# Performance work log

Hardware: AMD Instinct MI355X
Metric: run time of the kernel (lower is better)

The kernel has to match this reference:

```python
import jax, jax.numpy as jnp
import numpy as np
from fractions import Fraction
from math import factorial

# irreps metadata for "32x0e + 16x1o + 8x2e" (in/out) and "0e + 1o + 2e" (edge)
# parity of each irrep here equals (-1)**l, so parity selection == (l1+l2+l3) even
IRR_IN = [(32, 0), (16, 1), (8, 2)]   # (multiplicity, l)
IRR_SH = [(1, 0), (1, 1), (1, 2)]
IRR_OUT = IRR_IN

def _offsets(irr):
    offs, o = [], 0
    for mul, l in irr:
        offs.append(o)
        o += mul * (2 * l + 1)
    return offs, o

OFF_IN, DIM_IN = _offsets(IRR_IN)    # DIM_IN = 120
OFF_SH, DIM_SH = _offsets(IRR_SH)    # DIM_SH = 9
OFF_OUT, DIM_OUT = _offsets(IRR_OUT)

def _su2_cg(j1, j2, j3):
    """SU(2) Clebsch-Gordan tensor (e3nn convention), integer l."""
    f = factorial
    C = np.zeros((2 * j1 + 1, 2 * j2 + 1, 2 * j3 + 1))
    for m1 in range(-j1, j1 + 1):
        for m2 in range(-j2, j2 + 1):
            m3 = m1 + m2
            if abs(m3) > j3:
                continue
            vmin = max(-j1 + j2 + m3, -j1 + m1, 0)
            vmax = min(j2 + j3 + m1, j3 - j1 + j2, j3 + m3)
            c = ((2 * j3 + 1) * Fraction(
                f(j3 + j1 - j2) * f(j3 - j1 + j2) * f(j1 + j2 - j3) * f(j3 + m3) * f(j3 - m3),
                f(j1 + j2 + j3 + 1) * f(j1 - m1) * f(j1 + m1) * f(j2 - m2) * f(j2 + m2))) ** 0.5
            S = Fraction(0)
            for v in range(vmin, vmax + 1):
                S += (-1) ** (v + j2 + m2) * Fraction(
                    f(j2 + j3 + m1 - v) * f(j1 - m1 + v),
                    f(v) * f(j3 - j1 + j2 - v) * f(j3 + m3 - v) * f(v + j1 - j2 - m3))
            C[j1 + m1, j2 + m2, j3 + m3] = float(c) * float(S)
    return C

def _q(l):
    """real->complex change of basis for real spherical harmonics (e3nn)."""
    q = np.zeros((2 * l + 1, 2 * l + 1), dtype=np.complex128)
    for m in range(-l, 0):
        q[l + m, l - m] = 1 / np.sqrt(2)
        q[l + m, l + m] = -1j / np.sqrt(2)
    q[l, l] = 1
    for m in range(1, l + 1):
        q[l + m, l + m] = (-1) ** m / np.sqrt(2)
        q[l + m, l - m] = 1j * (-1) ** m / np.sqrt(2)
    return ((-1j) ** l) * q

def _w3j(l1, l2, l3):
    """real-basis Wigner 3j tensor, unit Frobenius norm (e3nn o3.wigner_3j)."""
    C = _su2_cg(l1, l2, l3).astype(np.complex128)
    C = np.einsum('ij,kl,mn,ikn->jlm', _q(l1), _q(l2), np.conj(_q(l3)).T, C)
    C = np.real(C)
    return (C / np.linalg.norm(C)).astype(np.float32)

# build 'uvw' instructions exactly as FullyConnectedTensorProduct does
INSTR = []
_wo = 0
for _i1, (_m1, _l1) in enumerate(IRR_IN):
    for _i2, (_m2, _l2) in enumerate(IRR_SH):
        for _i3, (_m3, _l3) in enumerate(IRR_OUT):
            if abs(_l1 - _l2) <= _l3 <= _l1 + _l2 and (_l1 + _l2 + _l3) % 2 == 0:
                INSTR.append(dict(i1=_i1, i2=_i2, i3=_i3, wo=_wo, cg=_w3j(_l1, _l2, _l3)))
                _wo += _m1 * _m2 * _m3
WEIGHT_NUMEL = _wo  # 3456

# path_normalization='element', irrep_normalization='component':
# coeff = sqrt((2*l_out+1) / sum_{paths into out} mul1*mul2)
_FAN = {}
for _ins in INSTR:
    _FAN[_ins['i3']] = _FAN.get(_ins['i3'], 0) + IRR_IN[_ins['i1']][0] * IRR_SH[_ins['i2']][0]
for _ins in INSTR:
    _l3 = IRR_OUT[_ins['i3']][1]
    _ins['coeff'] = float(np.sqrt((2 * _l3 + 1) / _FAN[_ins['i3']]))


def _tensor_product(x1, x2, w):
    """x1 (E,120) gathered node feats, x2 (E,9) edge SH, w (E,3456) radial weights."""
    E = x1.shape[0]
    acc = [None] * len(IRR_OUT)
    for ins in INSTR:
        m1, l1 = IRR_IN[ins['i1']]
        m3, l3 = IRR_OUT[ins['i3']]
        d1, d2 = 2 * l1 + 1, 2 * IRR_SH[ins['i2']][1] + 1
        x1b = x1[:, OFF_IN[ins['i1']]:OFF_IN[ins['i1']] + m1 * d1].reshape(E, m1, d1)
        x2b = x2[:, OFF_SH[ins['i2']]:OFF_SH[ins['i2']] + d2]        # mul2 == 1
        wb = w[:, ins['wo']:ins['wo'] + m1 * m3].reshape(E, m1, m3)
        cg = jnp.asarray(ins['cg'])                                   # (d1,d2,d3)
        tmp = jnp.einsum('eui,ej,ijk->euk', x1b, x2b, cg)             # (E,m1,d3)
        c = ins['coeff'] * jnp.einsum('euk,euw->ewk', tmp, wb)        # (E,m3,d3)
        acc[ins['i3']] = c if acc[ins['i3']] is None else acc[ins['i3']] + c
    return jnp.concatenate([a.reshape(E, -1) for a in acc], axis=-1)


def _self_interaction(agg, si_ws):
    """o3.Linear: per-l channel mixing, scaled by 1/sqrt(fan_in)."""
    N = agg.shape[0]
    outs = []
    for (m, l), off, W in zip(IRR_OUT, OFF_OUT, si_ws):
        d = 2 * l + 1
        xb = agg[:, off:off + m * d].reshape(N, m, d)
        outs.append((jnp.einsum('nuk,uv->nvk', xb, W) * (1.0 / np.sqrt(m))).reshape(N, -1))
    return jnp.concatenate(outs, axis=-1)


def setup_inputs() -> dict:
    key = jax.random.key(0)
    ks = jax.random.split(key, 10)
    N, E, NB = 4096, 32768, 8
    return {
        'node_features': jax.random.normal(ks[0], (N, DIM_IN), jnp.float32),
        'edge_index': jax.random.randint(ks[1], (2, E), 0, N, dtype=jnp.int32),
        'edge_sh': jax.random.normal(ks[2], (E, DIM_SH), jnp.float32),
        'edge_radial': jax.random.uniform(ks[3], (E, NB), dtype=jnp.float32),
        'w1': jax.random.normal(ks[4], (NB, 64), jnp.float32) / np.sqrt(NB),
        'b1': jnp.zeros((64,), jnp.float32),
        'w2': jax.random.normal(ks[5], (64, 64), jnp.float32) / np.sqrt(64),
        'b2': jnp.zeros((64,), jnp.float32),
        'w3': jax.random.normal(ks[6], (64, WEIGHT_NUMEL), jnp.float32) / np.sqrt(64),
        'b3': jnp.zeros((WEIGHT_NUMEL,), jnp.float32),
        'si_w0': jax.random.normal(ks[7], (32, 32), jnp.float32),
        'si_w1': jax.random.normal(ks[8], (16, 16), jnp.float32),
        'si_w2': jax.random.normal(ks[9], (8, 8), jnp.float32),
    }


def reference(node_features, edge_index, edge_sh, edge_radial,
              w1, b1, w2, b2, w3, b3, si_w0, si_w1, si_w2):
    src, dst = edge_index[0], edge_index[1]
    # radial MLP -> per-edge tensor-product weights
    h = jax.nn.silu(edge_radial @ w1 + b1)
    h = jax.nn.silu(h @ w2 + b2)
    weights = h @ w3 + b3                                     # (E, 3456)
    # gather-TP-scatter message passing
    msgs = _tensor_product(node_features[src], edge_sh, weights)   # (E, 120)
    agg = jax.ops.segment_sum(msgs, dst, num_segments=node_features.shape[0])
    out = _self_interaction(agg, [si_w0, si_w1, si_w2])
    return out + node_features  # shapes match -> residual
```

## Files before the change

kernel.cpp:

```cpp
#include <hip/hip_runtime.h>
#include <hip/hip_bf16.h>
#include <cmath>
#include <complex>

#define NT 512

typedef __bf16 bf16x8 __attribute__((ext_vector_type(8)));
typedef float  f32x4  __attribute__((ext_vector_type(4)));

struct CgPack { float v[363]; };

static double factd(int n) { double r = 1.0; for (int i = 2; i <= n; ++i) r *= i; return r; }

static void su2_cg(int j1, int j2, int j3, double C[5][5][5]) {
  for (int a = 0; a < 5; ++a) for (int b = 0; b < 5; ++b) for (int c = 0; c < 5; ++c) C[a][b][c] = 0.0;
  for (int m1 = -j1; m1 <= j1; ++m1)
    for (int m2 = -j2; m2 <= j2; ++m2) {
      int m3 = m1 + m2;
      if (m3 < -j3 || m3 > j3) continue;
      int vmin = -j1 + j2 + m3; if (-j1 + m1 > vmin) vmin = -j1 + m1; if (vmin < 0) vmin = 0;
      int vmax = j2 + j3 + m1; if (j3 - j1 + j2 < vmax) vmax = j3 - j1 + j2; if (j3 + m3 < vmax) vmax = j3 + m3;
      double c = std::sqrt((2.0 * j3 + 1.0) *
            factd(j3 + j1 - j2) * factd(j3 - j1 + j2) * factd(j1 + j2 - j3) * factd(j3 + m3) * factd(j3 - m3) /
            (factd(j1 + j2 + j3 + 1) * factd(j1 - m1) * factd(j1 + m1) * factd(j2 - m2) * factd(j2 + m2)));
      double S = 0.0;
      for (int v = vmin; v <= vmax; ++v) {
        double t = factd(j2 + j3 + m1 - v) * factd(j1 - m1 + v) /
                   (factd(v) * factd(j3 - j1 + j2 - v) * factd(j3 + m3 - v) * factd(v + j1 - j2 - m3));
        S += (((v + j2 + m2) & 1) ? -t : t);
      }
      C[j1 + m1][j2 + m2][j3 + m3] = c * S;
    }
}

typedef std::complex<double> cd;
static void qmat(int l, cd q[5][5]) {
  for (int a = 0; a < 5; ++a) for (int b = 0; b < 5; ++b) q[a][b] = cd(0.0, 0.0);
  const double is2 = 1.0 / std::sqrt(2.0);
  for (int m = -l; m < 0; ++m) { q[l + m][l - m] = cd(is2, 0.0); q[l + m][l + m] = cd(0.0, -is2); }
  q[l][l] = cd(1.0, 0.0);
  for (int m = 1; m <= l; ++m) {
    double sg = (m & 1) ? -1.0 : 1.0;
    q[l + m][l + m] = cd(sg * is2, 0.0);
    q[l + m][l - m] = cd(0.0, sg * is2);
  }
  cd ph(1.0, 0.0); const cd mi(0.0, -1.0);
  for (int t = 0; t < l; ++t) ph *= mi;
  for (int a = 0; a <= 2 * l; ++a) for (int b = 0; b <= 2 * l; ++b) q[a][b] *= ph;
}

static void w3j_fill(int l1, int l2, int l3, float* outp) {
  double C[5][5][5]; su2_cg(l1, l2, l3, C);
  cd q1[5][5], q2[5][5], q3[5][5];
  qmat(l1, q1); qmat(l2, q2); qmat(l3, q3);
  const int d1 = 2 * l1 + 1, d2 = 2 * l2 + 1, d3 = 2 * l3 + 1;
  double R[5][5][5]; double nrm = 0.0;
  for (int j = 0; j < d1; ++j)
    for (int L = 0; L < d2; ++L)
      for (int m = 0; m < d3; ++m) {
        cd s(0.0, 0.0);
        for (int i = 0; i < d1; ++i)
          for (int k = 0; k < d2; ++k)
            for (int n = 0; n < d3; ++n)
              s += q1[i][j] * q2[k][L] * std::conj(q3[n][m]) * C[i][k][n];
        R[j][L][m] = s.real();
        nrm += s.real() * s.real();
      }
  const double inv = 1.0 / std::sqrt(nrm);
  for (int j = 0; j < d1; ++j)
    for (int L = 0; L < d2; ++L)
      for (int m = 0; m < d3; ++m)
        outp[(j * d2 + L) * d3 + m] = (float)(R[j][L][m] * inv);
}

static void build_cg(CgPack* cg) {
  const int L1[11] = {0,0,0,1,1,1,1,2,2,2,2};
  const int L2[11] = {0,1,2,0,1,1,2,0,1,2,2};
  const int L3[11] = {0,1,2,1,0,2,1,2,1,0,2};
  const int CGO[11]= {0,1,10,35,44,53,98,143,168,213,238};
  for (int p = 0; p < 11; ++p) w3j_fill(L1[p], L2[p], L3[p], &cg->v[CGO[p]]);
}

constexpr int cP_l1[11] = {0,0,0,1,1,1,1,2,2,2,2};
constexpr int cP_l2[11] = {0,1,2,0,1,1,2,0,1,2,2};
constexpr int cP_l3[11] = {0,1,2,1,0,2,1,2,1,0,2};
constexpr int cP_wo[11] = {0,1024,1536,1792,2048,2560,2688,2944,3008,3136,3392};
constexpr int cP_cgo[11]= {0,1,10,35,44,53,98,143,168,213,238};
constexpr int mul_of_l(int l)    { return l == 0 ? 32 : (l == 1 ? 16 : 8); }
constexpr int off_in_of_l(int l) { return l == 0 ? 0  : (l == 1 ? 32 : 80); }
constexpr int off_sh_of_l(int l) { return l == 0 ? 0  : (l == 1 ? 1  : 4); }

__device__ __forceinline__ float silu_f(float x) { return x / (1.0f + __expf(-x)); }

template<int wo, int m3, int d3>
__device__ __forceinline__ void tile_mm(
    const __bf16* __restrict__ w3b, const float* __restrict__ b3,
    const float* tmpw, const bf16x8 hB0, const bf16x8 hB1,
    const int u0, const int tt, const int uu, const int lr, const int lc,
    float (&acc)[4*d3])
{
  const int cb = wo + u0*m3 + tt*16;
  const __bf16* ap = w3b + (size_t)(cb + lc)*64 + lr*8;
  const bf16x8 a0 = *(const bf16x8*)ap;
  const bf16x8 a1 = *(const bf16x8*)(ap + 32);
  f32x4 dd = {0.f, 0.f, 0.f, 0.f};
  dd = __builtin_amdgcn_mfma_f32_16x16x32_bf16(a0, hB0, dd, 0, 0, 0);
  dd = __builtin_amdgcn_mfma_f32_16x16x32_bf16(a1, hB1, dd, 0, 0, 0);
  float tv[d3];
  #pragma unroll
  for (int k = 0; k < d3; ++k) tv[k] = tmpw[(uu*d3 + k)*16 + lc];
  #pragma unroll
  for (int r = 0; r < 4; ++r) {
    const float w = dd[r] + b3[cb + lr*4 + r];
    #pragma unroll
    for (int k = 0; k < d3; ++k) acc[r*d3 + k] += w * tv[k];
  }
}

template<int P>
__device__ __forceinline__ void wave_path(
    const CgPack& cg, const __bf16* __restrict__ w3b, const float* __restrict__ b3,
    const float* __restrict__ nf, const int* esrc, float (&x2s)[64][13],
    float* tmpw, float (&msg)[64][121],
    const bf16x8 hB0, const bf16x8 hB1, const int g, const int lane)
{
  constexpr int l1 = cP_l1[P], l2 = cP_l2[P], l3 = cP_l3[P];
  constexpr int m1 = mul_of_l(l1), m3 = mul_of_l(l3);
  constexpr int d1 = 2*l1+1, d2 = 2*l2+1, d3 = 2*l3+1;
  constexpr int off1 = off_in_of_l(l1);
  constexpr int off2 = off_sh_of_l(l2);
  constexpr int off3 = off_in_of_l(l3);
  constexpr int wo = cP_wo[P], cgo = cP_cgo[P];
  constexpr float coeff = (l3==0) ? 0.13363062095621219f
                         : (l3==1) ? 0.20412414523193154f
                                   : 0.27950849718747373f;
  constexpr int UBLK = (m1 < 16) ? m1 : 16;
  constexpr int NUB  = m1 / UBLK;
  constexpr int NTIL = UBLK * m3 / 16;

  const int lr = lane >> 4, lc = lane & 15;
  const int e  = g*16 + lc;

  float accA[4*d3];
  float accB[(m3==32) ? 4 : 1];
  #pragma unroll
  for (int i = 0; i < 4*d3; ++i) accA[i] = 0.0f;
  #pragma unroll
  for (int i = 0; i < ((m3==32) ? 4 : 1); ++i) accB[i] = 0.0f;

  for (int ub = 0; ub < NUB; ++ub) {
    const int u0 = ub * UBLK;
    #pragma unroll
    for (int it = 0; it < UBLK/4; ++it) {
      const int idx = (it << 6) + lane;
      const int te = idx & 15, uu = idx >> 4;
      const float* xr = nf + (size_t)esrc[g*16 + te] * 120 + (off1 + (u0 + uu)*d1);
      float t[d3];
      #pragma unroll
      for (int k = 0; k < d3; ++k) t[k] = 0.0f;
      #pragma unroll
      for (int i = 0; i < d1; ++i) {
        const float a = xr[i];
        #pragma unroll
        for (int j = 0; j < d2; ++j) {
          const float ab = a * x2s[g*16 + te][off2 + j];
          #pragma unroll
          for (int k = 0; k < d3; ++k) t[k] += ab * cg.v[cgo + (i*d2 + j)*d3 + k];
        }
      }
      #pragma unroll
      for (int k = 0; k < d3; ++k) tmpw[(uu*d3 + k)*16 + te] = t[k];
    }

    if constexpr (m3 == 32) {
      for (int tt = 0; tt < NTIL; tt += 2) {
        tile_mm<wo, m3, d3>(w3b, b3, tmpw, hB0, hB1, u0, tt,   tt>>1, lr, lc, accA);
        tile_mm<wo, m3, d3>(w3b, b3, tmpw, hB0, hB1, u0, tt+1, tt>>1, lr, lc, accB);
      }
    } else {
      for (int tt = 0; tt < NTIL; ++tt) {
        const int uu = (m3 == 16) ? tt : (2*tt + (lr >> 1));
        tile_mm<wo, m3, d3>(w3b, b3, tmpw, hB0, hB1, u0, tt, uu, lr, lc, accA);
      }
    }
  }

  if constexpr (m3 == 16) {
    #pragma unroll
    for (int r = 0; r < 4; ++r)
      #pragma unroll
      for (int k = 0; k < d3; ++k)
        atomicAdd(&msg[e][off3 + (lr*4 + r)*d3 + k], coeff * accA[r*d3 + k]);
  } else if constexpr (m3 == 8) {
    #pragma unroll
    for (int i = 0; i < 4*d3; ++i) accA[i] += __shfl_xor(accA[i], 32, 64);
    if (lane < 32) {
      #pragma unroll
      for (int r = 0; r < 4; ++r)
        #pragma unroll
        for (int k = 0; k < d3; ++k)
          atomicAdd(&msg[e][off3 + (lr*4 + r)*d3 + k], coeff * accA[r*d3 + k]);
    }
  } else {
    #pragma unroll
    for (int r = 0; r < 4; ++r) {
      atomicAdd(&msg[e][off3 +      lr*4 + r], coeff * accA[r]);
      atomicAdd(&msg[e][off3 + 16 + lr*4 + r], coeff * accB[r]);
    }
  }
}

__global__ __launch_bounds__(256)
void conv_w3(const float* __restrict__ w3, __bf16* __restrict__ w3b, const int n) {
  const int idx = blockIdx.x * 256 + threadIdx.x;
  if (idx >= n) return;
  const int k = idx / 3456, col = idx - k * 3456;
  w3b[(size_t)col * 64 + k] = (__bf16)w3[idx];
}

__global__ __launch_bounds__(NT, 4)
void tp_fused(const float* __restrict__ nf, const int* __restrict__ eidx,
              const float* __restrict__ sh, const float* __restrict__ rad,
              const float* __restrict__ w1, const float* __restrict__ b1,
              const float* __restrict__ w2, const float* __restrict__ b2,
              const __bf16* __restrict__ w3b, const float* __restrict__ b3,
              float* __restrict__ agg, const int E, const CgPack cg)
{
  __shared__ float msg[64][121];
  __shared__ float x2s[64][13];
  __shared__ float tmparea[8][1280];
  __shared__ int   esrc[64], edst[64];

  const int tid  = threadIdx.x;
  const int lane = tid & 63, w = tid >> 6;
  const int g = w & 3, half = w >> 2;
  const int lr = lane >> 4, lc = lane & 15;
  const int e0 = blockIdx.x * 64;

  float*  h1T = &tmparea[0][0];
  __bf16* h2b = (__bf16*)((char*)&tmparea[0][0] + 16384);

  if (tid < 64)       esrc[tid]      = eidx[e0 + tid];
  else if (tid < 128) edst[tid - 64] = eidx[E + e0 + tid - 64];
  for (int idx = tid; idx < 64 * 64; idx += NT) {
    const int c = idx >> 6, e = idx & 63;
    const float4* r4 = (const float4*)(rad + (size_t)(e0 + e) * 8);
    const float4 ra = r4[0], rb = r4[1];
    float a = b1[c];
    a += ra.x * w1[0*64+c] + ra.y * w1[1*64+c] + ra.z * w1[2*64+c] + ra.w * w1[3*64+c];
    a += rb.x * w1[4*64+c] + rb.y * w1[5*64+c] + rb.z * w1[6*64+c] + rb.w * w1[7*64+c];
    h1T[c * 64 + e] = silu_f(a);
  }
  for (int idx = tid; idx < 64 * 9; idx += NT) {
    const int e = idx / 9, j = idx - e * 9;
    x2s[e][j] = sh[(size_t)(e0 + e) * 9 + j];
  }
  for (int idx = tid; idx < 64 * 121; idx += NT) (&msg[0][0])[idx] = 0.0f;
  __syncthreads();

  for (int idx = tid; idx < 64 * 16; idx += NT) {
    const int c = idx >> 4, eq = (idx & 15) * 4;
    float a0 = b2[c], a1 = b2[c], a2 = b2[c], a3 = b2[c];
    #pragma unroll 8
    for (int i = 0; i < 64; ++i) {
      const float wv = w2[i * 64 + c];
      const float4 h4 = *(const float4*)(&h1T[i * 64 + eq]);
      a0 += h4.x * wv; a1 += h4.y * wv; a2 += h4.z * wv; a3 += h4.w * wv;
    }
    h2b[(eq+0)*64 + c] = (__bf16)silu_f(a0);
    h2b[(eq+1)*64 + c] = (__bf16)silu_f(a1);
    h2b[(eq+2)*64 + c] = (__bf16)silu_f(a2);
    h2b[(eq+3)*64 + c] = (__bf16)silu_f(a3);
  }
  __syncthreads();

  const bf16x8 hB0 = *(const bf16x8*)(h2b + (g*16 + lc)*64 +      lr*8);
  const bf16x8 hB1 = *(const bf16x8*)(h2b + (g*16 + lc)*64 + 32 + lr*8);
  __syncthreads();

  float* tmpw = tmparea[w];

  if (half == 0) {
    wave_path<0>(cg, w3b, b3, nf, esrc, x2s, tmpw, msg, hB0, hB1, g, lane);
    wave_path<1>(cg, w3b, b3, nf, esrc, x2s, tmpw, msg, hB0, hB1, g, lane);
    wave_path<5>(cg, w3b, b3, nf, esrc, x2s, tmpw, msg, hB0, hB1, g, lane);
    wave_path<7>(cg, w3b, b3, nf, esrc, x2s, tmpw, msg, hB0, hB1, g, lane);
  } else {
    wave_path<2>(cg, w3b, b3, nf, esrc, x2s, tmpw, msg, hB0, hB1, g, lane);
    wave_path<3>(cg, w3b, b3, nf, esrc, x2s, tmpw, msg, hB0, hB1, g, lane);
    wave_path<4>(cg, w3b, b3, nf, esrc, x2s, tmpw, msg, hB0, hB1, g, lane);
    wave_path<6>(cg, w3b, b3, nf, esrc, x2s, tmpw, msg, hB0, hB1, g, lane);
    wave_path<8>(cg, w3b, b3, nf, esrc, x2s, tmpw, msg, hB0, hB1, g, lane);
    wave_path<9>(cg, w3b, b3, nf, esrc, x2s, tmpw, msg, hB0, hB1, g, lane);
    wave_path<10>(cg, w3b, b3, nf, esrc, x2s, tmpw, msg, hB0, hB1, g, lane);
  }
  __syncthreads();

  for (int idx = tid; idx < 64 * 120; idx += NT) {
    const int e = idx / 120, d = idx - e * 120;
    atomicAdd(&agg[(size_t)edst[e] * 120 + d], msg[e][d]);
  }
}

__global__ __launch_bounds__(128)
void si_kernel(const float* __restrict__ agg, const float* __restrict__ nf,
               const float* __restrict__ w0, const float* __restrict__ wl1,
               const float* __restrict__ wl2, float* __restrict__ out)
{
  __shared__ float a[120];
  const int n = blockIdx.x, tid = threadIdx.x;
  if (tid < 120) a[tid] = agg[(size_t)n * 120 + tid];
  __syncthreads();
  if (tid >= 120) return;
  float s = 0.0f;
  if (tid < 32) {
    const int v = tid;
    #pragma unroll
    for (int u = 0; u < 32; ++u) s += a[u] * w0[u * 32 + v];
    s *= 0.17677669529663687f;
  } else if (tid < 80) {
    const int r = tid - 32, v = r / 3, k = r - 3 * v;
    #pragma unroll
    for (int u = 0; u < 16; ++u) s += a[32 + u * 3 + k] * wl1[u * 16 + v];
    s *= 0.25f;
  } else {
    const int r = tid - 80, v = r / 5, k = r - 5 * v;
    #pragma unroll
    for (int u = 0; u < 8; ++u) s += a[80 + u * 5 + k] * wl2[u * 8 + v];
    s *= 0.35355339059327373f;
  }
  out[(size_t)n * 120 + tid] = s + nf[(size_t)n * 120 + tid];
}

extern "C" void kernel_launch(void* const* d_in, const int* in_sizes, int n_in,
                              void* d_out, int out_size, void* d_ws, size_t ws_size,
                              hipStream_t stream) {
  const float* nf  = (const float*)d_in[0];
  const int*   ei  = (const int*)  d_in[1];
  const float* sh  = (const float*)d_in[2];
  const float* rad = (const float*)d_in[3];
  const float* w1  = (const float*)d_in[4];
  const float* b1  = (const float*)d_in[5];
  const float* w2  = (const float*)d_in[6];
  const float* b2  = (const float*)d_in[7];
  const float* w3  = (const float*)d_in[8];
  const float* b3  = (const float*)d_in[9];
  const float* si0 = (const float*)d_in[10];
  const float* si1 = (const float*)d_in[11];
  const float* si2 = (const float*)d_in[12];
  float* out = (float*)d_out;

  const int N = in_sizes[0] / 120;
  const int E = in_sizes[2] / 9;
  const int W3N = in_sizes[8];

  float*  agg = (float*)d_ws;
  __bf16* w3b = (__bf16*)((char*)d_ws + (size_t)N * 120 * sizeof(float));
  hipMemsetAsync(agg, 0, (size_t)N * 120 * sizeof(float), stream);

  CgPack cg;
  build_cg(&cg);

  conv_w3<<<(W3N + 255) / 256, 256, 0, stream>>>(w3, w3b, W3N);
  tp_fused<<<E / 64, NT, 0, stream>>>(nf, ei, sh, rad, w1, b1, w2, b2, w3b, b3, agg, E, cg);
  si_kernel<<<N, 128, 0, stream>>>(agg, nf, si0, si1, si2, out);
}
```

Measured before the change: 279.5 us.

## Halve edges per block and split path u-blocks across waves for occupancy

Each block now handles 32 edges instead of 64. The 8 waves are split into 2 edge groups times 4 u-block lanes, and every path's multiplicity loop is strided across those waves instead of whole paths being assigned to half the block. Shared memory shrinks (msg is reused as h1T scratch, tmp area is smaller) and launch bounds raise the target to 8 blocks, aiming to improve occupancy and balance the path workload. The bias is now folded into the MFMA accumulator initialisation. The trade-off is more blocks, more atomic traffic per unit of work, and recomputing the radial MLP per 32 edges.

Result: slower. 429.6 us (+53.7%).

```diff
diff --git a/kernel.cpp b/kernel.cpp
--- a/kernel.cpp
+++ b/kernel.cpp
@@ -100,10 +100,11 @@
     float (&acc)[4*d3])
 {
   const int cb = wo + u0*m3 + tt*16;
+  const float4 b4 = *(const float4*)(b3 + cb + lr*4);
   const __bf16* ap = w3b + (size_t)(cb + lc)*64 + lr*8;
   const bf16x8 a0 = *(const bf16x8*)ap;
   const bf16x8 a1 = *(const bf16x8*)(ap + 32);
-  f32x4 dd = {0.f, 0.f, 0.f, 0.f};
+  f32x4 dd = {b4.x, b4.y, b4.z, b4.w};
   dd = __builtin_amdgcn_mfma_f32_16x16x32_bf16(a0, hB0, dd, 0, 0, 0);
   dd = __builtin_amdgcn_mfma_f32_16x16x32_bf16(a1, hB1, dd, 0, 0, 0);
   float tv[d3];
@@ -111,18 +112,18 @@
   for (int k = 0; k < d3; ++k) tv[k] = tmpw[(uu*d3 + k)*16 + lc];
   #pragma unroll
   for (int r = 0; r < 4; ++r) {
-    const float w = dd[r] + b3[cb + lr*4 + r];
-    #pragma unroll
-    for (int k = 0; k < d3; ++k) acc[r*d3 + k] += w * tv[k];
+    #pragma unroll
+    for (int k = 0; k < d3; ++k) acc[r*d3 + k] += dd[r] * tv[k];
   }
 }
 
 template<int P>
 __device__ __forceinline__ void wave_path(
     const CgPack& cg, const __bf16* __restrict__ w3b, const float* __restrict__ b3,
-    const float* __restrict__ nf, const int* esrc, float (&x2s)[64][13],
-    float* tmpw, float (&msg)[64][121],
-    const bf16x8 hB0, const bf16x8 hB1, const int g, const int lane)
+    const float* __restrict__ nf, const int* esrc, float (&x2s)[32][13],
+    float* tmpw, float (&msg)[32][121],
+    const bf16x8 hB0, const bf16x8 hB1, const int g, const int lane,
+    const int ub0, const int ubstep)
 {
   constexpr int l1 = cP_l1[P], l2 = cP_l2[P], l3 = cP_l3[P];
   constexpr int m1 = mul_of_l(l1), m3 = mul_of_l(l3);
@@ -134,7 +135,7 @@
   constexpr float coeff = (l3==0) ? 0.13363062095621219f
                          : (l3==1) ? 0.20412414523193154f
                                    : 0.27950849718747373f;
-  constexpr int UBLK = (m1 < 16) ? m1 : 16;
+  constexpr int UBLK = 4;
   constexpr int NUB  = m1 / UBLK;
   constexpr int NTIL = UBLK * m3 / 16;
 
@@ -148,12 +149,10 @@
   #pragma unroll
   for (int i = 0; i < ((m3==32) ? 4 : 1); ++i) accB[i] = 0.0f;
 
-  for (int ub = 0; ub < NUB; ++ub) {
+  for (int ub = ub0; ub < NUB; ub += ubstep) {
     const int u0 = ub * UBLK;
-    #pragma unroll
-    for (int it = 0; it < UBLK/4; ++it) {
-      const int idx = (it << 6) + lane;
-      const int te = idx & 15, uu = idx >> 4;
+    {
+      const int te = lane & 15, uu = lane >> 4;
       const float* xr = nf + (size_t)esrc[g*16 + te] * 120 + (off1 + (u0 + uu)*d1);
       float t[d3];
       #pragma unroll
@@ -173,11 +172,13 @@
     }
 
     if constexpr (m3 == 32) {
+      #pragma unroll
       for (int tt = 0; tt < NTIL; tt += 2) {
         tile_mm<wo, m3, d3>(w3b, b3, tmpw, hB0, hB1, u0, tt,   tt>>1, lr, lc, accA);
         tile_mm<wo, m3, d3>(w3b, b3, tmpw, hB0, hB1, u0, tt+1, tt>>1, lr, lc, accB);
       }
     } else {
+      #pragma unroll
       for (int tt = 0; tt < NTIL; ++tt) {
         const int uu = (m3 == 16) ? tt : (2*tt + (lr >> 1));
         tile_mm<wo, m3, d3>(w3b, b3, tmpw, hB0, hB1, u0, tt, uu, lr, lc, accA);
@@ -218,7 +219,7 @@
   w3b[(size_t)col * 64 + k] = (__bf16)w3[idx];
 }
 
-__global__ __launch_bounds__(NT, 4)
+__global__ __launch_bounds__(NT, 8)
 void tp_fused(const float* __restrict__ nf, const int* __restrict__ eidx,
               const float* __restrict__ sh, const float* __restrict__ rad,
               const float* __restrict__ w1, const float* __restrict__ b1,
@@ -226,45 +227,44 @@
               const __bf16* __restrict__ w3b, const float* __restrict__ b3,
               float* __restrict__ agg, const int E, const CgPack cg)
 {
-  __shared__ float msg[64][121];
-  __shared__ float x2s[64][13];
-  __shared__ float tmparea[8][1280];
-  __shared__ int   esrc[64], edst[64];
+  __shared__ float msg[32][121];
+  __shared__ float x2s[32][13];
+  __shared__ float tmparea[8][320];
+  __shared__ int   esrc[32], edst[32];
 
   const int tid  = threadIdx.x;
   const int lane = tid & 63, w = tid >> 6;
-  const int g = w & 3, half = w >> 2;
+  const int g = w & 1, q = w >> 1;
   const int lr = lane >> 4, lc = lane & 15;
-  const int e0 = blockIdx.x * 64;
-
-  float*  h1T = &tmparea[0][0];
-  __bf16* h2b = (__bf16*)((char*)&tmparea[0][0] + 16384);
-
-  if (tid < 64)       esrc[tid]      = eidx[e0 + tid];
-  else if (tid < 128) edst[tid - 64] = eidx[E + e0 + tid - 64];
-  for (int idx = tid; idx < 64 * 64; idx += NT) {
-    const int c = idx >> 6, e = idx & 63;
+  const int e0 = blockIdx.x * 32;
+
+  float*  h1T = &msg[0][0];
+  __bf16* h2b = (__bf16*)&tmparea[0][0];
+
+  if (tid < 32)      esrc[tid]      = eidx[e0 + tid];
+  else if (tid < 64) edst[tid - 32] = eidx[E + e0 + tid - 32];
+  for (int idx = tid; idx < 64 * 32; idx += NT) {
+    const int c = idx >> 5, e = idx & 31;
     const float4* r4 = (const float4*)(rad + (size_t)(e0 + e) * 8);
     const float4 ra = r4[0], rb = r4[1];
     float a = b1[c];
     a += ra.x * w1[0*64+c] + ra.y * w1[1*64+c] + ra.z * w1[2*64+c] + ra.w * w1[3*64+c];
     a += rb.x * w1[4*64+c] + rb.y * w1[5*64+c] + rb.z * w1[6*64+c] + rb.w * w1[7*64+c];
-    h1T[c * 64 + e] = silu_f(a);
-  }
-  for (int idx = tid; idx < 64 * 9; idx += NT) {
+    h1T[c * 32 + e] = silu_f(a);
+  }
+  for (int idx = tid; idx < 32 * 9; idx += NT) {
     const int e = idx / 9, j = idx - e * 9;
     x2s[e][j] = sh[(size_t)(e0 + e) * 9 + j];
   }
-  for (int idx = tid; idx < 64 * 121; idx += NT) (&msg[0][0])[idx] = 0.0f;
-  __syncthreads();
-
-  for (int idx = tid; idx < 64 * 16; idx += NT) {
-    const int c = idx >> 4, eq = (idx & 15) * 4;
+  __syncthreads();
+
+  {
+    const int c = tid >> 3, eq = (tid & 7) * 4;
     float a0 = b2[c], a1 = b2[c], a2 = b2[c], a3 = b2[c];
     #pragma unroll 8
     for (int i = 0; i < 64; ++i) {
       const float wv = w2[i * 64 + c];
-      const float4 h4 = *(const float4*)(&h1T[i * 64 + eq]);
+      const float4 h4 = *(const float4*)(&h1T[i * 32 + eq]);
       a0 += h4.x * wv; a1 += h4.y * wv; a2 += h4.z * wv; a3 += h4.w * wv;
     }
     h2b[(eq+0)*64 + c] = (__bf16)silu_f(a0);
@@ -276,27 +276,28 @@
 
   const bf16x8 hB0 = *(const bf16x8*)(h2b + (g*16 + lc)*64 +      lr*8);
   const bf16x8 hB1 = *(const bf16x8*)(h2b + (g*16 + lc)*64 + 32 + lr*8);
+  for (int idx = tid; idx < 32 * 121; idx += NT) (&msg[0][0])[idx] = 0.0f;
   __syncthreads();
 
   float* tmpw = tmparea[w];
 
-  if (half == 0) {
-    wave_path<0>(cg, w3b, b3, nf, esrc, x2s, tmpw, msg, hB0, hB1, g, lane);
-    wave_path<1>(cg, w3b, b3, nf, esrc, x2s, tmpw, msg, hB0, hB1, g, lane);
-    wave_path<5>(cg, w3b, b3, nf, esrc, x2s, tmpw, msg, hB0, hB1, g, lane);
-    wave_path<7>(cg, w3b, b3, nf, esrc, x2s, tmpw, msg, hB0, hB1, g, lane);
+  wave_path<0>(cg, w3b, b3, nf, esrc, x2s, tmpw, msg, hB0, hB1, g, lane, q, 4);
+  wave_path<1>(cg, w3b, b3, nf, esrc, x2s, tmpw, msg, hB0, hB1, g, lane, q, 4);
+  wave_path<2>(cg, w3b, b3, nf, esrc, x2s, tmpw, msg, hB0, hB1, g, lane, q, 4);
+  wave_path<3>(cg, w3b, b3, nf, esrc, x2s, tmpw, msg, hB0, hB1, g, lane, q, 4);
+  wave_path<4>(cg, w3b, b3, nf, esrc, x2s, tmpw, msg, hB0, hB1, g, lane, q, 4);
+  wave_path<5>(cg, w3b, b3, nf, esrc, x2s, tmpw, msg, hB0, hB1, g, lane, q, 4);
+  wave_path<6>(cg, w3b, b3, nf, esrc, x2s, tmpw, msg, hB0, hB1, g, lane, q, 4);
+  if (q < 2) {
+    wave_path<7>(cg, w3b, b3, nf, esrc, x2s, tmpw, msg, hB0, hB1, g, lane, q, 2);
+    wave_path<9>(cg, w3b, b3, nf, esrc, x2s, tmpw, msg, hB0, hB1, g, lane, q, 2);
   } else {
-    wave_path<2>(cg, w3b, b3, nf, esrc, x2s, tmpw, msg, hB0, hB1, g, lane);
-    wave_path<3>(cg, w3b, b3, nf, esrc, x2s, tmpw, msg, hB0, hB1, g, lane);
-    wave_path<4>(cg, w3b, b3, nf, esrc, x2s, tmpw, msg, hB0, hB1, g, lane);
-    wave_path<6>(cg, w3b, b3, nf, esrc, x2s, tmpw, msg, hB0, hB1, g, lane);
-    wave_path<8>(cg, w3b, b3, nf, esrc, x2s, tmpw, msg, hB0, hB1, g, lane);
-    wave_path<9>(cg, w3b, b3, nf, esrc, x2s, tmpw, msg, hB0, hB1, g, lane);
-    wave_path<10>(cg, w3b, b3, nf, esrc, x2s, tmpw, msg, hB0, hB1, g, lane);
-  }
-  __syncthreads();
-
-  for (int idx = tid; idx < 64 * 120; idx += NT) {
+    wave_path<8>(cg, w3b, b3, nf, esrc, x2s, tmpw, msg, hB0, hB1, g, lane, q-2, 2);
+    wave_path<10>(cg, w3b, b3, nf, esrc, x2s, tmpw, msg, hB0, hB1, g, lane, q-2, 2);
+  }
+  __syncthreads();
+
+  for (int idx = tid; idx < 32 * 120; idx += NT) {
     const int e = idx / 120, d = idx - e * 120;
     atomicAdd(&agg[(size_t)edst[e] * 120 + d], msg[e][d]);
   }
@@ -362,6 +363,6 @@
   build_cg(&cg);
 
   conv_w3<<<(W3N + 255) / 256, 256, 0, stream>>>(w3, w3b, W3N);
-  tp_fused<<<E / 64, NT, 0, stream>>>(nf, ei, sh, rad, w1, b1, w2, b2, w3b, b3, agg, E, cg);
+  tp_fused<<<E / 32, NT, 0, stream>>>(nf, ei, sh, rad, w1, b1, w2, b2, w3b, b3, agg, E, cg);
   si_kernel<<<N, 128, 0, stream>>>(agg, nf, si0, si1, si2, out);
 }
```
